# Kernel tuning notes

Measured on AMD Instinct MI355X. Metric: run time of the kernel, lower is better.

The kernel has to match this reference:

```python
import jax, jax.numpy as jnp
import numpy as np

B, T, D = 64, 256, 1024
H, HS = 16, 64
FF = 4096
EPS = 1e-5


def _layernorm(x, g, b):
    mu = jnp.mean(x, axis=-1, keepdims=True)
    var = jnp.mean(jnp.square(x - mu), axis=-1, keepdims=True)
    return (x - mu) * jax.lax.rsqrt(var + EPS) * g + b


def setup_inputs() -> dict:
    key = jax.random.key(0)
    ks = jax.random.split(key, 12)
    s = 0.02
    return {
        "x": jax.random.normal(ks[0], (B, T, D), jnp.float32),
        "ln1_g": jnp.ones((D,), jnp.float32),
        "ln1_b": jnp.zeros((D,), jnp.float32),
        "Wq": jax.random.normal(ks[1], (H, D, HS), jnp.float32) * s,
        "Wk": jax.random.normal(ks[2], (H, D, HS), jnp.float32) * s,
        "Wv": jax.random.normal(ks[3], (H, D, HS), jnp.float32) * s,
        "Wproj": jax.random.normal(ks[4], (D, D), jnp.float32) * s,
        "bproj": jnp.zeros((D,), jnp.float32),
        "ln2_g": jnp.ones((D,), jnp.float32),
        "ln2_b": jnp.zeros((D,), jnp.float32),
        "W1": jax.random.normal(ks[5], (D, FF), jnp.float32) * s,
        "b1": jnp.zeros((FF,), jnp.float32),
        "W2": jax.random.normal(ks[6], (FF, D), jnp.float32) * s,
        "b2": jnp.zeros((D,), jnp.float32),
    }


def reference(x, ln1_g, ln1_b, Wq, Wk, Wv, Wproj, bproj, ln2_g, ln2_b, W1, b1, W2, b2):
    # x = ln1(x)
    h = _layernorm(x, ln1_g, ln1_b)
    # per-head Q/K/V projections, batched over heads
    q = jnp.einsum("btd,hde->bhte", h, Wq)
    k = jnp.einsum("btd,hde->bhte", h, Wk)
    v = jnp.einsum("btd,hde->bhte", h, Wv)
    # NOTE: source scales by C**-0.5 with C = input_size (D), not head_size
    scale = D ** -0.5
    scores = jnp.einsum("bhte,bhse->bhts", q, k) * scale
    causal = jnp.tril(jnp.ones((T, T), bool))
    scores = jnp.where(causal, scores, -jnp.inf)
    w = jax.nn.softmax(scores, axis=-1)  # dropout is identity in eval
    attn = jnp.einsum("bhts,bhse->bthe", w, v).reshape(x.shape[0], x.shape[1], H * HS)
    sa = attn @ Wproj + bproj
    # residual onto ln1 output (as written in source)
    y = h + sa
    h2 = _layernorm(y, ln2_g, ln2_b)
    ff = jax.nn.relu(h2 @ W1 + b1) @ W2 + b2
    return h2 + ff
```

## Files before the change

### kernel.cpp

```cpp
#include <hip/hip_runtime.h>

typedef __bf16 bf16x8 __attribute__((ext_vector_type(8)));
typedef float f32x4 __attribute__((ext_vector_type(4)));
typedef unsigned short ushort_t;

__device__ __forceinline__ ushort_t f2bf(float f) {
  unsigned int u = __float_as_uint(f);
  u += 0x7fffu + ((u >> 16) & 1u);
  return (ushort_t)(u >> 16);
}
__device__ __forceinline__ float bf2f(ushort_t u) {
  return __uint_as_float(((unsigned int)u) << 16);
}

__device__ __forceinline__ void gl_lds16(const ushort_t* g, const char* l) {
  __builtin_amdgcn_global_load_lds(
      (const __attribute__((address_space(1))) void*)g,
      (__attribute__((address_space(3))) void*)l, 16, 0, 0);
}

__global__ __launch_bounds__(256) void fill_k(float* __restrict__ p, long n, float v) {
  long i = (long)blockIdx.x * 256 + threadIdx.x;
  if (i < n) p[i] = v;
}

__global__ __launch_bounds__(256) void transpose_w(const float* __restrict__ in,
                                                   ushort_t* __restrict__ out,
                                                   int R, int C) {
  __shared__ float tile[32][33];
  const float* inb = in + (long)blockIdx.z * R * C;
  ushort_t* outb = out + (long)blockIdx.z * R * C;
  int r0 = blockIdx.x * 32, c0 = blockIdx.y * 32;
  int tx = threadIdx.x & 31, ty = threadIdx.x >> 5;
#pragma unroll
  for (int i = ty; i < 32; i += 8) tile[i][tx] = inb[(long)(r0 + i) * C + (c0 + tx)];
  __syncthreads();
#pragma unroll
  for (int i = ty; i < 32; i += 8) outb[(long)(c0 + i) * R + (r0 + tx)] = f2bf(tile[tx][i]);
}

template <bool BFIN>
__global__ __launch_bounds__(256) void ln_k(const void* __restrict__ xin,
                                            const float* __restrict__ g,
                                            const float* __restrict__ b,
                                            ushort_t* __restrict__ outU) {
  __shared__ float red[8];
  long row = blockIdx.x;
  int tid = threadIdx.x;
  float4 v;
  if constexpr (BFIN) {
    ushort4 u4 = ((const ushort4*)((const ushort_t*)xin + row * 1024))[tid];
    v = make_float4(bf2f(u4.x), bf2f(u4.y), bf2f(u4.z), bf2f(u4.w));
  } else {
    v = ((const float4*)((const float*)xin + row * 1024))[tid];
  }
  float s = v.x + v.y + v.z + v.w;
#pragma unroll
  for (int off = 32; off; off >>= 1) s += __shfl_xor(s, off);
  int w = tid >> 6;
  if ((tid & 63) == 0) red[w] = s;
  __syncthreads();
  float mean = (red[0] + red[1] + red[2] + red[3]) * (1.0f / 1024.0f);
  float dx = v.x - mean, dy = v.y - mean, dz = v.z - mean, dw = v.w - mean;
  float s2 = dx * dx + dy * dy + dz * dz + dw * dw;
#pragma unroll
  for (int off = 32; off; off >>= 1) s2 += __shfl_xor(s2, off);
  if ((tid & 63) == 0) red[4 + w] = s2;
  __syncthreads();
  float var = (red[4] + red[5] + red[6] + red[7]) * (1.0f / 1024.0f);
  float rstd = rsqrtf(var + 1e-5f);
  int c = tid * 4;
  ushort4 u;
  u.x = f2bf(dx * rstd * g[c + 0] + b[c + 0]);
  u.y = f2bf(dy * rstd * g[c + 1] + b[c + 1]);
  u.z = f2bf(dz * rstd * g[c + 2] + b[c + 2]);
  u.w = f2bf(dw * rstd * g[c + 3] + b[c + 3]);
  ((ushort4*)(outU + row * 1024))[tid] = u;
}

template <int EPI>
__global__ __launch_bounds__(512, 2) void gemm256(const ushort_t* __restrict__ A,
                                                  const ushort_t* __restrict__ Bt,
                                                  int M, int N, int K, int NBC,
                                                  const float* __restrict__ bias,
                                                  const ushort_t* __restrict__ resU,
                                                  float* __restrict__ outF,
                                                  ushort_t* __restrict__ outU,
                                                  ushort_t* __restrict__ outU2,
                                                  ushort_t* __restrict__ outU3) {
  __shared__ __align__(16) char lds[131072];
  const int tid = threadIdx.x;
  const int lane = tid & 63;
  const int w = tid >> 6;
  const int wr = w >> 2, wc = w & 3;
  const int g = lane >> 4, lr = lane & 15;
  const int cpx = gridDim.x >> 3;
  const int wg = (blockIdx.x & 7) * cpx + (blockIdx.x >> 3);
  const int NBM = gridDim.x / NBC;
  const long m0 = (long)(wg % NBM) * 256;
  const long n0 = (long)(wg / NBM) * 256;
  const int srow = tid >> 3;
  const int sslot = (tid & 7) ^ (srow & 7);
  const ushort_t* sA = A + (m0 + srow) * (long)K + sslot * 8;
  const ushort_t* sB = Bt + (n0 + srow) * (long)K + sslot * 8;
  const int dA = tid * 16;
  const int dB = 32768 + tid * 16;
  const int abase = (wr * 128 + lr) * 128;
  const int bbase = 32768 + (wc * 64 + lr) * 128;
  const int s0 = g ^ (lr & 7);
  const int s1 = (4 + g) ^ (lr & 7);
  const int NT = K >> 6;

  f32x4 acc[8][4] = {};
  bf16x8 aR[8][2], bR[4][2];
  const char* rb;

#define STAGE_TILE(tile) do {                                             \
    const long _ko = (long)(tile) * 64;                                   \
    char* _d = lds + (((tile) & 1) << 16);                                \
    gl_lds16(sA + _ko, _d + dA);                                          \
    gl_lds16(sA + _ko + 64 * (long)K, _d + 8192 + dA);                    \
    gl_lds16(sA + _ko + 128 * (long)K, _d + 16384 + dA);                  \
    gl_lds16(sA + _ko + 192 * (long)K, _d + 24576 + dA);                  \
    gl_lds16(sB + _ko, _d + dB);                                          \
    gl_lds16(sB + _ko + 64 * (long)K, _d + 8192 + dB);                    \
    gl_lds16(sB + _ko + 128 * (long)K, _d + 16384 + dB);                  \
    gl_lds16(sB + _ko + 192 * (long)K, _d + 24576 + dB);                  \
  } while (0)
#define RD_ALL do {                                                       \
    _Pragma("unroll") for (int mf = 0; mf < 8; ++mf) {                    \
      aR[mf][0] = *(const bf16x8*)(rb + abase + mf * 2048 + s0 * 16);     \
      aR[mf][1] = *(const bf16x8*)(rb + abase + mf * 2048 + s1 * 16);     \
    }                                                                     \
    _Pragma("unroll") for (int nf = 0; nf < 4; ++nf) {                    \
      bR[nf][0] = *(const bf16x8*)(rb + bbase + nf * 2048 + s0 * 16);     \
      bR[nf][1] = *(const bf16x8*)(rb + bbase + nf * 2048 + s1 * 16);     \
    } } while (0)
#define QUAD32(NB) do {                                                   \
    __builtin_amdgcn_s_setprio(1);                                        \
    _Pragma("unroll") for (int mf = 0; mf < 8; ++mf)                      \
      _Pragma("unroll") for (int nf = 0; nf < 2; ++nf) {                  \
        acc[mf][(NB) + nf] = __builtin_amdgcn_mfma_f32_16x16x32_bf16(aR[mf][0], bR[(NB) + nf][0], acc[mf][(NB) + nf], 0, 0, 0); \
        acc[mf][(NB) + nf] = __builtin_amdgcn_mfma_f32_16x16x32_bf16(aR[mf][1], bR[(NB) + nf][1], acc[mf][(NB) + nf], 0, 0, 0); \
      }                                                                   \
    __builtin_amdgcn_s_setprio(0); } while (0)
#define LGKM0 do {                                                        \
    asm volatile("s_waitcnt lgkmcnt(0)" ::: "memory");                    \
    __builtin_amdgcn_sched_barrier(0); } while (0)

  STAGE_TILE(0);
  STAGE_TILE(1);
  asm volatile("s_waitcnt vmcnt(8)" ::: "memory");
  __builtin_amdgcn_s_barrier();

  int c = 0;
  for (int t = 0; t < NT; ++t) {
    rb = lds + c;
    RD_ALL;
    __builtin_amdgcn_s_barrier();
    LGKM0;
    QUAD32(0);
    __builtin_amdgcn_s_barrier();
    if (t + 2 < NT) STAGE_TILE(t + 2);
    QUAD32(2);
    if (t + 2 < NT) asm volatile("s_waitcnt vmcnt(8)" ::: "memory");
    else            asm volatile("s_waitcnt vmcnt(0)" ::: "memory");
    __builtin_amdgcn_s_barrier();
    c ^= 65536;
  }
#undef STAGE_TILE
#undef RD_ALL
#undef QUAD32
#undef LGKM0

  if constexpr (EPI == 3 || EPI == 5) {
    ushort_t* l16 = (ushort_t*)lds;
#pragma unroll
    for (int mf = 0; mf < 8; ++mf)
#pragma unroll
      for (int nf = 0; nf < 4; ++nf) {
        int col = wc * 64 + nf * 16 + lr;
        long gcol = n0 + col;
#pragma unroll
        for (int r = 0; r < 4; ++r) {
          int row = wr * 128 + mf * 16 + g * 4 + r;
          float v = acc[mf][nf][r] + bias[gcol];
          if constexpr (EPI == 3) v = fmaxf(v, 0.0f);
          else v += bf2f(resU[(m0 + row) * (long)N + gcol]);
          l16[row * 256 + (col ^ (g << 3))] = f2bf(v);
        }
      }
    __syncthreads();
#pragma unroll
    for (int k = 0; k < 16; ++k) {
      int c2 = tid + k * 512;
      int tt = c2 >> 5, off = c2 & 31;
      int pc = (off * 8) ^ ((((unsigned)tt >> 2) & 3) << 3);
      uint4 d = *(uint4*)&l16[tt * 256 + pc];
      *(uint4*)&outU[(m0 + tt) * (long)N + n0 + off * 8] = d;
    }
  } else if constexpr (EPI == 6) {
#pragma unroll
    for (int mf = 0; mf < 8; ++mf)
#pragma unroll
      for (int nf = 0; nf < 4; ++nf)
#pragma unroll
        for (int r = 0; r < 4; ++r) {
          long row = m0 + wr * 128 + mf * 16 + g * 4 + r;
          long col = n0 + wc * 64 + nf * 16 + lr;
          long i = row * (long)N + col;
          outF[i] = acc[mf][nf][r] + bias[col] + bf2f(resU[i]);
        }
  } else {
    const int p = (int)(n0 >> 10);
    const long bb2 = m0 >> 8;
    if (p < 2) {
      ushort_t* dst = (p == 0) ? outU : outU2;
      ushort_t* l16 = (ushort_t*)lds;
#pragma unroll
      for (int mf = 0; mf < 8; ++mf)
#pragma unroll
        for (int nf = 0; nf < 4; ++nf) {
          int col = wc * 64 + nf * 16 + lr;
#pragma unroll
          for (int r = 0; r < 4; ++r) {
            int row = wr * 128 + mf * 16 + g * 4 + r;
            l16[row * 256 + (col ^ (g << 3))] = f2bf(acc[mf][nf][r]);
          }
        }
      __syncthreads();
      const int hh0 = (int)((n0 & 1023) >> 6);
#pragma unroll
      for (int k = 0; k < 16; ++k) {
        int c2 = tid + k * 512;
        int hh_l = c2 >> 11, tt = (c2 >> 3) & 255, off = c2 & 7;
        int col = hh_l * 64 + off * 8;
        int pc = col ^ ((((unsigned)tt >> 2) & 3) << 3);
        uint4 d = *(uint4*)&l16[tt * 256 + pc];
        *(uint4*)&dst[(((bb2 * 16 + hh0 + hh_l) * 256 + tt) << 6) + off * 8] = d;
      }
    } else {
      unsigned int* l32 = (unsigned int*)lds;
#pragma unroll
      for (int mf = 0; mf < 8; ++mf)
#pragma unroll
        for (int nf = 0; nf < 4; ++nf)
#pragma unroll
          for (int r2 = 0; r2 < 2; ++r2) {
            int row = wr * 128 + mf * 16 + g * 4 + r2 * 2;
            int col = wc * 64 + nf * 16 + lr;
            unsigned int pk = (unsigned int)f2bf(acc[mf][nf][r2 * 2]) |
                              ((unsigned int)f2bf(acc[mf][nf][r2 * 2 + 1]) << 16);
            l32[col * 128 + ((row >> 1) ^ ((col & 7) << 2))] = pk;
          }
      __syncthreads();
      const long vcol0 = (n0 & 1023);
#pragma unroll
      for (int k = 0; k < 16; ++k) {
        int c2 = tid + k * 512;
        int e_l = c2 >> 5, k16 = c2 & 31;
        uint4 d = *(uint4*)&l32[e_l * 128 + ((k16 * 4) ^ ((e_l & 7) << 2))];
        long vc = vcol0 + e_l;
        long hh = vc >> 6, e = vc & 63;
        *(uint4*)&outU3[(((bb2 * 16 + hh) * 64 + e) << 8) + k16 * 8] = d;
      }
    }
  }
}

__global__ __launch_bounds__(64, 4) void attn_k(const ushort_t* __restrict__ q,
                                                const ushort_t* __restrict__ k,
                                                const ushort_t* __restrict__ vt,
                                                ushort_t* __restrict__ ao) {
  __shared__ __align__(16) ushort_t Ps[32][40];
  const int lane = threadIdx.x;
  const int g = lane >> 4, lr = lane & 15;
  const int blk = blockIdx.x;
  const int q8 = blk & 7;
  const int bh = blk >> 3;
  const int bb = bh >> 4, hh = bh & 15;
  const int q0 = q8 * 32;
  const ushort_t* qb = q + (long)bh * 256 * 64;
  const ushort_t* kb = k + (long)bh * 256 * 64;
  const ushort_t* vb = vt + (long)bh * 64 * 256;
  bf16x8 qf[2][2];
#pragma unroll
  for (int m = 0; m < 2; m++)
#pragma unroll
    for (int ks = 0; ks < 2; ks++)
      qf[m][ks] = *(const bf16x8*)(qb + (q0 + m * 16 + lr) * 64 + ks * 32 + g * 8);
  f32x4 o[2][4] = {};
  float mrow[2][4], lrow[2][4];
#pragma unroll
  for (int m = 0; m < 2; m++)
#pragma unroll
    for (int r = 0; r < 4; r++) { mrow[m][r] = -3.0e38f; lrow[m][r] = 0.0f; }
  const float sc2 = 0.04508422f;
  const int nkb = q8 + 1;
  for (int kbk = 0; kbk < nkb; kbk++) {
    f32x4 s[2][2] = {};
#pragma unroll
    for (int ks = 0; ks < 2; ks++) {
      bf16x8 kf[2];
#pragma unroll
      for (int n = 0; n < 2; n++)
        kf[n] = *(const bf16x8*)(kb + (kbk * 32 + n * 16 + lr) * 64 + ks * 32 + g * 8);
#pragma unroll
      for (int m = 0; m < 2; m++)
#pragma unroll
        for (int n = 0; n < 2; n++)
          s[m][n] = __builtin_amdgcn_mfma_f32_16x16x32_bf16(qf[m][ks], kf[n], s[m][n], 0, 0, 0);
    }
    bf16x8 vf[4];
#pragma unroll
    for (int n = 0; n < 4; n++)
      vf[n] = *(const bf16x8*)(vb + (n * 16 + lr) * 256 + kbk * 32 + g * 8);
    if (kbk == q8) {
#pragma unroll
      for (int m = 0; m < 2; m++)
#pragma unroll
        for (int n = 0; n < 2; n++)
#pragma unroll
          for (int r = 0; r < 4; r++) {
            int row = q0 + m * 16 + g * 4 + r;
            int col = kbk * 32 + n * 16 + lr;
            s[m][n][r] = (col <= row) ? s[m][n][r] * sc2 : -3.0e38f;
          }
    } else {
#pragma unroll
      for (int m = 0; m < 2; m++)
#pragma unroll
        for (int n = 0; n < 2; n++)
#pragma unroll
          for (int r = 0; r < 4; r++) s[m][n][r] *= sc2;
    }
    float mx[2][4];
    float growth = -3.0e38f;
#pragma unroll
    for (int m = 0; m < 2; m++)
#pragma unroll
      for (int r = 0; r < 4; r++) {
        float v = fmaxf(s[m][0][r], s[m][1][r]);
#pragma unroll
        for (int off = 8; off; off >>= 1) v = fmaxf(v, __shfl_xor(v, off));
        mx[m][r] = v;
        growth = fmaxf(growth, v - mrow[m][r]);
      }
    if (__any(growth > 8.0f)) {
#pragma unroll
      for (int m = 0; m < 2; m++)
#pragma unroll
        for (int r = 0; r < 4; r++) {
          float mn = fmaxf(mrow[m][r], mx[m][r]);
          float al = exp2f(mrow[m][r] - mn);
          mrow[m][r] = mn;
          lrow[m][r] *= al;
#pragma unroll
          for (int n = 0; n < 4; n++) o[m][n][r] *= al;
        }
    }
#pragma unroll
    for (int m = 0; m < 2; m++)
#pragma unroll
      for (int r = 0; r < 4; r++) {
        float rs = 0.0f;
#pragma unroll
        for (int n = 0; n < 2; n++) {
          float p = exp2f(s[m][n][r] - mrow[m][r]);
          s[m][n][r] = p;
          rs += p;
        }
#pragma unroll
        for (int off = 8; off; off >>= 1) rs += __shfl_xor(rs, off);
        lrow[m][r] += rs;
      }
#pragma unroll
    for (int m = 0; m < 2; m++)
#pragma unroll
      for (int n = 0; n < 2; n++)
#pragma unroll
        for (int r = 0; r < 4; r++)
          Ps[m * 16 + g * 4 + r][n * 16 + lr] = f2bf(s[m][n][r]);
#pragma unroll
    for (int m = 0; m < 2; m++) {
      bf16x8 pa = *(const bf16x8*)&Ps[m * 16 + lr][g * 8];
#pragma unroll
      for (int n = 0; n < 4; n++)
        o[m][n] = __builtin_amdgcn_mfma_f32_16x16x32_bf16(pa, vf[n], o[m][n], 0, 0, 0);
    }
  }
#pragma unroll
  for (int m = 0; m < 2; m++)
#pragma unroll
    for (int r = 0; r < 4; r++) {
      float inv = 1.0f / lrow[m][r];
      long t = q0 + m * 16 + g * 4 + r;
#pragma unroll
      for (int n = 0; n < 4; n++) {
        long e = n * 16 + lr;
        ao[((long)bb * 256 + t) * 1024 + hh * 64 + e] = f2bf(o[m][n][r] * inv);
      }
    }
}

extern "C" void kernel_launch(void* const* d_in, const int* in_sizes, int n_in,
                              void* d_out, int out_size, void* d_ws, size_t ws_size,
                              hipStream_t stream) {
  const float* x     = (const float*)d_in[0];
  const float* ln1g  = (const float*)d_in[1];
  const float* ln1b  = (const float*)d_in[2];
  const float* Wq    = (const float*)d_in[3];
  const float* Wk    = (const float*)d_in[4];
  const float* Wv    = (const float*)d_in[5];
  const float* Wproj = (const float*)d_in[6];
  const float* bproj = (const float*)d_in[7];
  const float* ln2g  = (const float*)d_in[8];
  const float* ln2b  = (const float*)d_in[9];
  const float* W1    = (const float*)d_in[10];
  const float* b1    = (const float*)d_in[11];
  const float* W2    = (const float*)d_in[12];
  const float* b2    = (const float*)d_in[13];

  const long NEED = 184L << 20;
  if (ws_size < (size_t)NEED) {
    fill_k<<<(out_size + 255) / 256, 256, 0, stream>>>((float*)d_out, out_size,
                                                       (float)(ws_size >> 20));
    return;
  }

  char* ws = (char*)d_ws;
  const long MB = 1 << 20;
  ushort_t* wqt = (ushort_t*)(ws + 0 * MB);
  ushort_t* wkt = (ushort_t*)(ws + 2 * MB);
  ushort_t* wvt = (ushort_t*)(ws + 4 * MB);
  ushort_t* wpt = (ushort_t*)(ws + 6 * MB);
  ushort_t* w1t = (ushort_t*)(ws + 8 * MB);
  ushort_t* w2t = (ushort_t*)(ws + 16 * MB);
  ushort_t* hb  = (ushort_t*)(ws + 24 * MB);
  ushort_t* qbf = (ushort_t*)(ws + 56 * MB);
  ushort_t* kbf = (ushort_t*)(ws + 88 * MB);
  ushort_t* vtb = (ushort_t*)(ws + 120 * MB);
  ushort_t* atb = (ushort_t*)(ws + 152 * MB);
  ushort_t* yb  = (ushort_t*)(ws + 56 * MB);
  ushort_t* ff1 = (ushort_t*)(ws + 56 * MB);

  transpose_w<<<dim3(32, 2, 16), 256, 0, stream>>>(Wq, wqt, 1024, 64);
  transpose_w<<<dim3(32, 2, 16), 256, 0, stream>>>(Wk, wkt, 1024, 64);
  transpose_w<<<dim3(32, 2, 16), 256, 0, stream>>>(Wv, wvt, 1024, 64);
  transpose_w<<<dim3(32, 32, 1), 256, 0, stream>>>(Wproj, wpt, 1024, 1024);
  transpose_w<<<dim3(32, 128, 1), 256, 0, stream>>>(W1, w1t, 1024, 4096);
  transpose_w<<<dim3(128, 32, 1), 256, 0, stream>>>(W2, w2t, 4096, 1024);

  ln_k<false><<<16384, 256, 0, stream>>>(x, ln1g, ln1b, hb);
  gemm256<4><<<768, 512, 0, stream>>>(hb, wqt, 16384, 3072, 1024, 12,
                                      nullptr, nullptr, nullptr, qbf, kbf, vtb);
  attn_k<<<8192, 64, 0, stream>>>(qbf, kbf, vtb, atb);
  gemm256<5><<<256, 512, 0, stream>>>(atb, wpt, 16384, 1024, 1024, 4,
                                      bproj, hb, nullptr, yb, nullptr, nullptr);
  ln_k<true><<<16384, 256, 0, stream>>>(yb, ln2g, ln2b, hb);
  gemm256<3><<<1024, 512, 0, stream>>>(hb, w1t, 16384, 4096, 1024, 16,
                                       b1, nullptr, nullptr, ff1, nullptr, nullptr);
  gemm256<6><<<256, 512, 0, stream>>>(ff1, w2t, 16384, 1024, 4096, 4,
                                      b2, hb, (float*)d_out, nullptr, nullptr, nullptr);
}
```

Before: 604.0 us.

## Shrink GEMM tile to 256x128 with K=32 steps for higher occupancy

The shared GEMM kernel moves from 256x256 output tiles with K=64 double buffering to 256x128 tiles with K=32 steps. That cuts LDS use from 128 KB to about 48 KB and raises launch bounds to allow 4 blocks per CU. Each wave now computes 64x64 with fewer accumulator registers, and grid sizes double to match. The aim is more occupancy and more blocks to fill the CUs. In exchange, arithmetic intensity per tile drops and there are more barriers per unit of work, since each K step is shorter.

```diff
diff --git a/kernel.cpp b/kernel.cpp
--- a/kernel.cpp
+++ b/kernel.cpp
@@ -79,7 +79,7 @@
 }
 
 template <int EPI>
-__global__ __launch_bounds__(512, 2) void gemm256(const ushort_t* __restrict__ A,
+__global__ __launch_bounds__(512, 4) void gemm256(const ushort_t* __restrict__ A,
                                                   const ushort_t* __restrict__ Bt,
                                                   int M, int N, int K, int NBC,
                                                   const float* __restrict__ bias,
@@ -88,126 +88,104 @@
                                                   ushort_t* __restrict__ outU,
                                                   ushort_t* __restrict__ outU2,
                                                   ushort_t* __restrict__ outU3) {
-  __shared__ __align__(16) char lds[131072];
+  __shared__ __align__(16) char lds[65536];
   const int tid = threadIdx.x;
   const int lane = tid & 63;
   const int w = tid >> 6;
-  const int wr = w >> 2, wc = w & 3;
+  const int wm = w >> 1, wn = w & 1;
   const int g = lane >> 4, lr = lane & 15;
   const int cpx = gridDim.x >> 3;
   const int wg = (blockIdx.x & 7) * cpx + (blockIdx.x >> 3);
-  const int NBM = gridDim.x / NBC;
-  const long m0 = (long)(wg % NBM) * 256;
-  const long n0 = (long)(wg / NBM) * 256;
-  const int srow = tid >> 3;
-  const int sslot = (tid & 7) ^ (srow & 7);
+  const long m0 = (long)(wg / NBC) * 256;
+  const long n0 = (long)(wg % NBC) * 128;
+  const int srow = tid >> 2;
+  const int sslot = (tid & 3) ^ ((tid >> 3) & 3);
   const ushort_t* sA = A + (m0 + srow) * (long)K + sslot * 8;
   const ushort_t* sB = Bt + (n0 + srow) * (long)K + sslot * 8;
-  const int dA = tid * 16;
-  const int dB = 32768 + tid * 16;
-  const int abase = (wr * 128 + lr) * 128;
-  const int bbase = 32768 + (wc * 64 + lr) * 128;
-  const int s0 = g ^ (lr & 7);
-  const int s1 = (4 + g) ^ (lr & 7);
-  const int NT = K >> 6;
-
-  f32x4 acc[8][4] = {};
-  bf16x8 aR[8][2], bR[4][2];
-  const char* rb;
-
-#define STAGE_TILE(tile) do {                                             \
-    const long _ko = (long)(tile) * 64;                                   \
-    char* _d = lds + (((tile) & 1) << 16);                                \
-    gl_lds16(sA + _ko, _d + dA);                                          \
-    gl_lds16(sA + _ko + 64 * (long)K, _d + 8192 + dA);                    \
-    gl_lds16(sA + _ko + 128 * (long)K, _d + 16384 + dA);                  \
-    gl_lds16(sA + _ko + 192 * (long)K, _d + 24576 + dA);                  \
-    gl_lds16(sB + _ko, _d + dB);                                          \
-    gl_lds16(sB + _ko + 64 * (long)K, _d + 8192 + dB);                    \
-    gl_lds16(sB + _ko + 128 * (long)K, _d + 16384 + dB);                  \
-    gl_lds16(sB + _ko + 192 * (long)K, _d + 24576 + dB);                  \
+  const int dT = tid * 16;
+  const int swz = (g ^ ((lr >> 1) & 3)) * 16;
+  const int aoff = (wm * 64 + lr) * 64 + swz;
+  const int boff = 16384 + (wn * 64 + lr) * 64 + swz;
+  const int NT = K >> 5;
+
+  f32x4 acc[4][4] = {};
+  bf16x8 aR[4], bR[4];
+
+#define STAGE(tile) do {                                                  \
+    const long _ko = (long)(tile) * 32;                                   \
+    char* _d = lds + (((tile) & 1) ? 24576 : 0);                          \
+    gl_lds16(sA + _ko, _d + dT);                                          \
+    gl_lds16(sA + _ko + 128 * (long)K, _d + 8192 + dT);                   \
+    gl_lds16(sB + _ko, _d + 16384 + dT);                                  \
   } while (0)
-#define RD_ALL do {                                                       \
-    _Pragma("unroll") for (int mf = 0; mf < 8; ++mf) {                    \
-      aR[mf][0] = *(const bf16x8*)(rb + abase + mf * 2048 + s0 * 16);     \
-      aR[mf][1] = *(const bf16x8*)(rb + abase + mf * 2048 + s1 * 16);     \
-    }                                                                     \
-    _Pragma("unroll") for (int nf = 0; nf < 4; ++nf) {                    \
-      bR[nf][0] = *(const bf16x8*)(rb + bbase + nf * 2048 + s0 * 16);     \
-      bR[nf][1] = *(const bf16x8*)(rb + bbase + nf * 2048 + s1 * 16);     \
-    } } while (0)
-#define QUAD32(NB) do {                                                   \
-    __builtin_amdgcn_s_setprio(1);                                        \
-    _Pragma("unroll") for (int mf = 0; mf < 8; ++mf)                      \
-      _Pragma("unroll") for (int nf = 0; nf < 2; ++nf) {                  \
-        acc[mf][(NB) + nf] = __builtin_amdgcn_mfma_f32_16x16x32_bf16(aR[mf][0], bR[(NB) + nf][0], acc[mf][(NB) + nf], 0, 0, 0); \
-        acc[mf][(NB) + nf] = __builtin_amdgcn_mfma_f32_16x16x32_bf16(aR[mf][1], bR[(NB) + nf][1], acc[mf][(NB) + nf], 0, 0, 0); \
-      }                                                                   \
-    __builtin_amdgcn_s_setprio(0); } while (0)
-#define LGKM0 do {                                                        \
-    asm volatile("s_waitcnt lgkmcnt(0)" ::: "memory");                    \
-    __builtin_amdgcn_sched_barrier(0); } while (0)
-
-  STAGE_TILE(0);
-  STAGE_TILE(1);
-  asm volatile("s_waitcnt vmcnt(8)" ::: "memory");
+
+  STAGE(0);
+  STAGE(1);
+  asm volatile("s_waitcnt vmcnt(3)" ::: "memory");
   __builtin_amdgcn_s_barrier();
 
-  int c = 0;
   for (int t = 0; t < NT; ++t) {
-    rb = lds + c;
-    RD_ALL;
+    const char* rb = lds + ((t & 1) ? 24576 : 0);
+#pragma unroll
+    for (int mf = 0; mf < 4; ++mf)
+      aR[mf] = *(const bf16x8*)(rb + aoff + mf * 1024);
+#pragma unroll
+    for (int nf = 0; nf < 4; ++nf)
+      bR[nf] = *(const bf16x8*)(rb + boff + nf * 1024);
+    asm volatile("s_waitcnt lgkmcnt(0)" ::: "memory");
+    __builtin_amdgcn_sched_barrier(0);
     __builtin_amdgcn_s_barrier();
-    LGKM0;
-    QUAD32(0);
-    __builtin_amdgcn_s_barrier();
-    if (t + 2 < NT) STAGE_TILE(t + 2);
-    QUAD32(2);
-    if (t + 2 < NT) asm volatile("s_waitcnt vmcnt(8)" ::: "memory");
-    else            asm volatile("s_waitcnt vmcnt(0)" ::: "memory");
-    __builtin_amdgcn_s_barrier();
-    c ^= 65536;
+    if (t + 2 < NT) STAGE(t + 2);
+    __builtin_amdgcn_s_setprio(1);
+#pragma unroll
+    for (int mf = 0; mf < 4; ++mf)
+#pragma unroll
+      for (int nf = 0; nf < 4; ++nf)
+        acc[mf][nf] = __builtin_amdgcn_mfma_f32_16x16x32_bf16(aR[mf], bR[nf], acc[mf][nf], 0, 0, 0);
+    __builtin_amdgcn_s_setprio(0);
+    if (t + 1 < NT) {
+      if (t + 2 < NT) asm volatile("s_waitcnt vmcnt(3)" ::: "memory");
+      else            asm volatile("s_waitcnt vmcnt(0)" ::: "memory");
+      __builtin_amdgcn_s_barrier();
+    }
   }
-#undef STAGE_TILE
-#undef RD_ALL
-#undef QUAD32
-#undef LGKM0
+#undef STAGE
 
   if constexpr (EPI == 3 || EPI == 5) {
     ushort_t* l16 = (ushort_t*)lds;
 #pragma unroll
-    for (int mf = 0; mf < 8; ++mf)
+    for (int mf = 0; mf < 4; ++mf)
 #pragma unroll
       for (int nf = 0; nf < 4; ++nf) {
-        int col = wc * 64 + nf * 16 + lr;
+        int col = wn * 64 + nf * 16 + lr;
         long gcol = n0 + col;
 #pragma unroll
         for (int r = 0; r < 4; ++r) {
-          int row = wr * 128 + mf * 16 + g * 4 + r;
+          int row = wm * 64 + mf * 16 + g * 4 + r;
           float v = acc[mf][nf][r] + bias[gcol];
           if constexpr (EPI == 3) v = fmaxf(v, 0.0f);
           else v += bf2f(resU[(m0 + row) * (long)N + gcol]);
-          l16[row * 256 + (col ^ (g << 3))] = f2bf(v);
+          l16[row * 128 + (col ^ (g << 3))] = f2bf(v);
         }
       }
     __syncthreads();
 #pragma unroll
-    for (int k = 0; k < 16; ++k) {
+    for (int k = 0; k < 8; ++k) {
       int c2 = tid + k * 512;
-      int tt = c2 >> 5, off = c2 & 31;
+      int tt = c2 >> 4, off = c2 & 15;
       int pc = (off * 8) ^ ((((unsigned)tt >> 2) & 3) << 3);
-      uint4 d = *(uint4*)&l16[tt * 256 + pc];
+      uint4 d = *(uint4*)&l16[tt * 128 + pc];
       *(uint4*)&outU[(m0 + tt) * (long)N + n0 + off * 8] = d;
     }
   } else if constexpr (EPI == 6) {
 #pragma unroll
-    for (int mf = 0; mf < 8; ++mf)
+    for (int mf = 0; mf < 4; ++mf)
 #pragma unroll
       for (int nf = 0; nf < 4; ++nf)
 #pragma unroll
         for (int r = 0; r < 4; ++r) {
-          long row = m0 + wr * 128 + mf * 16 + g * 4 + r;
-          long col = n0 + wc * 64 + nf * 16 + lr;
+          long row = m0 + wm * 64 + mf * 16 + g * 4 + r;
+          long col = n0 + wn * 64 + nf * 16 + lr;
           long i = row * (long)N + col;
           outF[i] = acc[mf][nf][r] + bias[col] + bf2f(resU[i]);
         }
@@ -218,37 +196,37 @@
       ushort_t* dst = (p == 0) ? outU : outU2;
       ushort_t* l16 = (ushort_t*)lds;
 #pragma unroll
-      for (int mf = 0; mf < 8; ++mf)
+      for (int mf = 0; mf < 4; ++mf)
 #pragma unroll
         for (int nf = 0; nf < 4; ++nf) {
-          int col = wc * 64 + nf * 16 + lr;
+          int col = wn * 64 + nf * 16 + lr;
 #pragma unroll
           for (int r = 0; r < 4; ++r) {
-            int row = wr * 128 + mf * 16 + g * 4 + r;
-            l16[row * 256 + (col ^ (g << 3))] = f2bf(acc[mf][nf][r]);
+            int row = wm * 64 + mf * 16 + g * 4 + r;
+            l16[row * 128 + (col ^ (g << 3))] = f2bf(acc[mf][nf][r]);
           }
         }
       __syncthreads();
       const int hh0 = (int)((n0 & 1023) >> 6);
 #pragma unroll
-      for (int k = 0; k < 16; ++k) {
+      for (int k = 0; k < 8; ++k) {
         int c2 = tid + k * 512;
-        int hh_l = c2 >> 11, tt = (c2 >> 3) & 255, off = c2 & 7;
-        int col = hh_l * 64 + off * 8;
-        int pc = col ^ ((((unsigned)tt >> 2) & 3) << 3);
-        uint4 d = *(uint4*)&l16[tt * 256 + pc];
-        *(uint4*)&dst[(((bb2 * 16 + hh0 + hh_l) * 256 + tt) << 6) + off * 8] = d;
+        int tt = c2 >> 4, off = c2 & 15;
+        int hh_l = off >> 3;
+        int pc = (off * 8) ^ ((((unsigned)tt >> 2) & 3) << 3);
+        uint4 d = *(uint4*)&l16[tt * 128 + pc];
+        *(uint4*)&dst[(((bb2 * 16 + hh0 + hh_l) * 256 + tt) << 6) + (off & 7) * 8] = d;
       }
     } else {
       unsigned int* l32 = (unsigned int*)lds;
 #pragma unroll
-      for (int mf = 0; mf < 8; ++mf)
+      for (int mf = 0; mf < 4; ++mf)
 #pragma unroll
         for (int nf = 0; nf < 4; ++nf)
 #pragma unroll
           for (int r2 = 0; r2 < 2; ++r2) {
-            int row = wr * 128 + mf * 16 + g * 4 + r2 * 2;
-            int col = wc * 64 + nf * 16 + lr;
+            int row = wm * 64 + mf * 16 + g * 4 + r2 * 2;
+            int col = wn * 64 + nf * 16 + lr;
             unsigned int pk = (unsigned int)f2bf(acc[mf][nf][r2 * 2]) |
                               ((unsigned int)f2bf(acc[mf][nf][r2 * 2 + 1]) << 16);
             l32[col * 128 + ((row >> 1) ^ ((col & 7) << 2))] = pk;
@@ -256,7 +234,7 @@
       __syncthreads();
       const long vcol0 = (n0 & 1023);
 #pragma unroll
-      for (int k = 0; k < 16; ++k) {
+      for (int k = 0; k < 8; ++k) {
         int c2 = tid + k * 512;
         int e_l = c2 >> 5, k16 = c2 & 31;
         uint4 d = *(uint4*)&l32[e_l * 128 + ((k16 * 4) ^ ((e_l & 7) << 2))];
@@ -452,14 +430,14 @@
   transpose_w<<<dim3(128, 32, 1), 256, 0, stream>>>(W2, w2t, 4096, 1024);
 
   ln_k<false><<<16384, 256, 0, stream>>>(x, ln1g, ln1b, hb);
-  gemm256<4><<<768, 512, 0, stream>>>(hb, wqt, 16384, 3072, 1024, 12,
-                                      nullptr, nullptr, nullptr, qbf, kbf, vtb);
+  gemm256<4><<<1536, 512, 0, stream>>>(hb, wqt, 16384, 3072, 1024, 24,
+                                       nullptr, nullptr, nullptr, qbf, kbf, vtb);
   attn_k<<<8192, 64, 0, stream>>>(qbf, kbf, vtb, atb);
-  gemm256<5><<<256, 512, 0, stream>>>(atb, wpt, 16384, 1024, 1024, 4,
+  gemm256<5><<<512, 512, 0, stream>>>(atb, wpt, 16384, 1024, 1024, 8,
                                       bproj, hb, nullptr, yb, nullptr, nullptr);
   ln_k<true><<<16384, 256, 0, stream>>>(yb, ln2g, ln2b, hb);
-  gemm256<3><<<1024, 512, 0, stream>>>(hb, w1t, 16384, 4096, 1024, 16,
+  gemm256<3><<<2048, 512, 0, stream>>>(hb, w1t, 16384, 4096, 1024, 32,
                                        b1, nullptr, nullptr, ff1, nullptr, nullptr);
-  gemm256<6><<<256, 512, 0, stream>>>(ff1, w2t, 16384, 1024, 4096, 4,
+  gemm256<6><<<512, 512, 0, stream>>>(ff1, w2t, 16384, 1024, 4096, 8,
                                       b2, hb, (float*)d_out, nullptr, nullptr, nullptr);
 }
```

After: 622.0 us. 3.0% more time.
